# Performance work log

Hardware: AMD Instinct MI355X
Metric: run time of the kernel (lower is better)

## Reference

```python
import jax, jax.numpy as jnp
import numpy as np

EPS = 1e-5

def _bn(h, gamma, beta):
    # BatchNorm1d in training mode: batch stats over dim 0, biased variance
    mu = h.mean(axis=0)
    var = ((h - mu) ** 2).mean(axis=0)
    return gamma * (h - mu) * jax.lax.rsqrt(var + EPS) + beta

def _gnn_layer(x, w, src, dst, Wv, bv, We, be, g_n, b_n, g_e, b_e):
    n_nodes = x.shape[0]
    # 4 node linears: Wv [4,d,d], bv [4,d]
    xl = jnp.einsum('nd,kfd->knf', x, Wv) + bv[:, None, :]  # [4, N, d]
    x1, x2, x3, x4 = xl[0], xl[1], xl[2], xl[3]
    # sigmoid-gated messages, mean-aggregated to source nodes
    msg = jax.nn.sigmoid(w) * x2[dst]                         # [E, d]
    agg = jax.ops.segment_sum(msg, src, num_segments=n_nodes)
    cnt = jax.ops.segment_sum(jnp.ones((src.shape[0], 1), x.dtype), src,
                              num_segments=n_nodes)
    agg = agg / jnp.maximum(cnt, 1.0)
    x_new = x + jax.nn.silu(_bn(x1 + agg, g_n, b_n))
    w_new = w + jax.nn.silu(_bn(w @ We.T + be + x3[src] + x4[dst], g_e, b_e))
    return x_new, w_new

def setup_inputs() -> dict:
    key = jax.random.key(0)
    N, E, D, L = 50000, 800000, 64, 3
    ks = jax.random.split(key, 10)
    x = jax.random.normal(ks[0], (N, D), dtype=jnp.float32)
    edge_index = jax.random.randint(ks[1], (2, E), 0, N, dtype=jnp.int64)
    edge_attr = jax.random.normal(ks[2], (E, D), dtype=jnp.float32)
    Wv = jax.random.normal(ks[3], (L, 4, D, D), dtype=jnp.float32) * 0.05
    bv = jax.random.normal(ks[4], (L, 4, D), dtype=jnp.float32) * 0.05
    We = jax.random.normal(ks[5], (L, D, D), dtype=jnp.float32) * 0.05
    be = jax.random.normal(ks[6], (L, D), dtype=jnp.float32) * 0.05
    g_node = jnp.ones((L, D), dtype=jnp.float32)
    b_node = jnp.zeros((L, D), dtype=jnp.float32)
    g_edge = jnp.ones((L, D), dtype=jnp.float32)
    b_edge = jnp.zeros((L, D), dtype=jnp.float32)
    return {"x": x, "edge_index": edge_index, "edge_attr": edge_attr,
            "Wv": Wv, "bv": bv, "We": We, "be": be,
            "g_node": g_node, "b_node": b_node,
            "g_edge": g_edge, "b_edge": b_edge}

def reference(x, edge_index, edge_attr, Wv, bv, We, be,
              g_node, b_node, g_edge, b_edge):
    src, dst = edge_index[0], edge_index[1]
    h = jax.nn.silu(x)
    w = jax.nn.silu(edge_attr)
    L = Wv.shape[0]
    for l in range(L):
        h, w = _gnn_layer(h, w, src, dst, Wv[l], bv[l], We[l], be[l],
                          g_node[l], b_node[l], g_edge[l], b_edge[l])
    return h, w
```

## Files before the change

kernel.cpp:

```cpp
#include <hip/hip_runtime.h>

#define NN 50000
#define NE 800000
#define EPSB 1e-5f

typedef __attribute__((ext_vector_type(8))) short bf16x8;
typedef __attribute__((ext_vector_type(8))) unsigned short ushort8;
typedef __attribute__((ext_vector_type(4))) float f32x4;

__device__ __forceinline__ float sigm(float x){ return 1.0f/(1.0f+__expf(-x)); }
__device__ __forceinline__ float silu_(float x){ return x/(1.0f+__expf(-x)); }
__device__ __forceinline__ unsigned int cvt2(float lo, float hi){
  unsigned int r;
  asm("v_cvt_pk_bf16_f32 %0, %1, %2" : "=v"(r) : "v"(lo), "v"(hi));
  return r;
}
__device__ __forceinline__ unsigned short f2bf(float x){
  return (unsigned short)cvt2(x, 0.f);
}
__device__ __forceinline__ float bf2f(unsigned short b){
  return __uint_as_float(((unsigned int)b)<<16);
}
__device__ __forceinline__ ushort8 pack8(float a0,float a1,float a2,float a3,
                                         float a4,float a5,float a6,float a7){
  union { unsigned int u[4]; ushort8 s; } z;
  z.u[0]=cvt2(a0,a1); z.u[1]=cvt2(a2,a3); z.u[2]=cvt2(a4,a5); z.u[3]=cvt2(a6,a7);
  return z.s;
}
__device__ __forceinline__ ushort8 sum8(ushort8 a, ushort8 b){
  return pack8(bf2f(a[0])+bf2f(b[0]), bf2f(a[1])+bf2f(b[1]),
               bf2f(a[2])+bf2f(b[2]), bf2f(a[3])+bf2f(b[3]),
               bf2f(a[4])+bf2f(b[4]), bf2f(a[5])+bf2f(b[5]),
               bf2f(a[6])+bf2f(b[6]), bf2f(a[7])+bf2f(b[7]));
}


__global__ __launch_bounds__(256) void k_deg(const int* __restrict__ src,
                                             int* __restrict__ deg){
  int e = blockIdx.x*256 + threadIdx.x;
  if (e < NE) atomicAdd(&deg[src[e]], 1);
}

__global__ __launch_bounds__(1024) void k_scan(const int* __restrict__ deg,
    int* __restrict__ cursor, float* __restrict__ invd){
  __shared__ int wsum[16];
  __shared__ int sbase;
  if (threadIdx.x == 0) sbase = 0;
  __syncthreads();
  const int lane = threadIdx.x & 63, wid = threadIdx.x >> 6;
  for (int start = 0; start < NN; start += 1024){
    int n = start + (int)threadIdx.x;
    int v = (n < NN) ? deg[n] : 0;
    int x = v;
    #pragma unroll
    for (int d=1; d<64; d<<=1){
      int y = __shfl_up(x, d);
      if (lane >= d) x += y;
    }
    if (lane == 63) wsum[wid] = x;
    __syncthreads();
    if (threadIdx.x < 16){
      int s = wsum[threadIdx.x];
      #pragma unroll
      for (int d=1; d<16; d<<=1){
        int y = __shfl_up(s, d);
        if ((int)threadIdx.x >= d) s += y;
      }
      wsum[threadIdx.x] = s;
    }
    __syncthreads();
    int excl = sbase + ((wid>0)? wsum[wid-1] : 0) + (x - v);
    if (n < NN){
      cursor[n] = excl;
      invd[n] = 1.0f / fmaxf((float)v, 1.0f);
    }
    __syncthreads();
    if (threadIdx.x == 0) sbase += wsum[15];
    __syncthreads();
  }
}

__global__ __launch_bounds__(256) void k_scatter(const int* __restrict__ src,
    const int* __restrict__ dst, int* __restrict__ cursor,
    int* __restrict__ perm, int* __restrict__ ssrc, int* __restrict__ sdst){
  int e = blockIdx.x*256 + threadIdx.x;
  if (e < NE){
    int s = src[e];
    int pos = atomicAdd(&cursor[s], 1);
    perm[pos] = e;
    ssrc[pos] = s;
    sdst[pos] = dst[e];
  }
}

__global__ __launch_bounds__(256) void k_prepW(const float* __restrict__ Wv,
    const float* __restrict__ We,
    unsigned short* __restrict__ wvs, unsigned short* __restrict__ wes){
  const int m = blockIdx.x;
  const float* S = (m < 12) ? (Wv + m*4096) : (We + (m-12)*4096);
  unsigned short* O = (m < 12) ? (wvs + m*4096) : (wes + (m-12)*4096);
  int t = threadIdx.x;
  #pragma unroll
  for (int p=0; p<2; ++p){
    int c = t + p*256;
    int row = c>>3, cc = c&7;
    const float4* sp = (const float4*)(S + row*64 + cc*8);
    float4 a = sp[0], b = sp[1];
    ushort8 v = pack8(a.x,a.y,a.z,a.w,b.x,b.y,b.z,b.w);
    *(ushort8*)((char*)O + ((row*128 + cc*16) ^ ((row&7)<<4))) = v;
  }
}

template<int MODE>
__global__ __launch_bounds__(256) void k_nodelin(const float* __restrict__ xin,
    float* __restrict__ h, float* __restrict__ x1, float* __restrict__ agg,
    const float* __restrict__ invd, const float* __restrict__ coefp,
    const unsigned short* __restrict__ wvs, const float* __restrict__ bvl,
    unsigned short* __restrict__ xb){
  __shared__ unsigned short shb[4096];
  __shared__ unsigned short sW[4096];
  const int n0 = blockIdx.x*64;
  const int t = threadIdx.x;
  #pragma unroll
  for (int p=0; p<2; ++p){
    int c = t + p*256;
    int row = c>>3, cc = c&7;
    int n = n0 + row;
    ushort8 v = {0,0,0,0,0,0,0,0};
    if (n < NN){
      unsigned base = (unsigned)n*64u + (unsigned)cc*8u;
      float4 a, b;
      if (MODE == 0){
        const float4* xp = (const float4*)(xin + base);
        a = xp[0]; b = xp[1];
        a.x=silu_(a.x); a.y=silu_(a.y); a.z=silu_(a.z); a.w=silu_(a.w);
        b.x=silu_(b.x); b.y=silu_(b.y); b.z=silu_(b.z); b.w=silu_(b.w);
        float4* hp = (float4*)(h + base);
        hp[0] = a; hp[1] = b;
      } else {
        float4* hp = (float4*)(h + base);
        a = hp[0]; b = hp[1];
        const float4* xp = (const float4*)(x1 + base);
        float4* gp = (float4*)(agg + base);
        float iv = invd[n];
        float4 xa = xp[0], xb4 = xp[1], ga = gp[0], gb = gp[1];
        float4 z = make_float4(0.f,0.f,0.f,0.f);
        gp[0] = z; gp[1] = z;
        float4 s0 = *(const float4*)(coefp + cc*8);
        float4 s1v = *(const float4*)(coefp + cc*8 + 4);
        float4 h0 = *(const float4*)(coefp + 64 + cc*8);
        float4 h1 = *(const float4*)(coefp + 64 + cc*8 + 4);
        a.x += silu_((xa.x + ga.x*iv)*s0.x + h0.x);
        a.y += silu_((xa.y + ga.y*iv)*s0.y + h0.y);
        a.z += silu_((xa.z + ga.z*iv)*s0.z + h0.z);
        a.w += silu_((xa.w + ga.w*iv)*s0.w + h0.w);
        b.x += silu_((xb4.x + gb.x*iv)*s1v.x + h1.x);
        b.y += silu_((xb4.y + gb.y*iv)*s1v.y + h1.y);
        b.z += silu_((xb4.z + gb.z*iv)*s1v.z + h1.z);
        b.w += silu_((xb4.w + gb.w*iv)*s1v.w + h1.w);
        hp[0] = a; hp[1] = b;
      }
      v = pack8(a.x,a.y,a.z,a.w,b.x,b.y,b.z,b.w);
    }
    *(ushort8*)((char*)shb + ((row*128 + cc*16) ^ ((row&7)<<4))) = v;
  }
  __syncthreads();
  const int wid = t>>6, lane = t&63, g = lane>>4, ln = lane&15;
  const int arow = wid*16 + ln;
  bf16x8 afr0 = *(bf16x8*)((char*)shb + ((arow*128 +  0 + g*16) ^ ((arow&7)<<4)));
  bf16x8 afr1 = *(bf16x8*)((char*)shb + ((arow*128 + 64 + g*16) ^ ((arow&7)<<4)));
  for (int k=0; k<4; ++k){
    __syncthreads();
    ((ushort8*)sW)[t]     = ((const ushort8*)(wvs + k*4096))[t];
    ((ushort8*)sW)[t+256] = ((const ushort8*)(wvs + k*4096))[t+256];
    __syncthreads();
    #pragma unroll
    for (int ft=0; ft<4; ++ft){
      int brow = ft*16 + ln;
      bf16x8 b0 = *(bf16x8*)((char*)sW + ((brow*128 +  0 + g*16) ^ ((brow&7)<<4)));
      bf16x8 b1 = *(bf16x8*)((char*)sW + ((brow*128 + 64 + g*16) ^ ((brow&7)<<4)));
      f32x4 c = {0.f,0.f,0.f,0.f};
      c = __builtin_amdgcn_mfma_f32_16x16x32_bf16(afr0, b0, c, 0,0,0);
      c = __builtin_amdgcn_mfma_f32_16x16x32_bf16(afr1, b1, c, 0,0,0);
      float bias = bvl[k*64 + brow];
      #pragma unroll
      for (int r=0; r<4; ++r){
        int n = n0 + wid*16 + g*4 + r;
        if (n < NN){
          float val = c[r] + bias;
          unsigned off = (unsigned)n*64u + (unsigned)brow;
          if (k == 0) x1[off] = val;
          else xb[(unsigned)(k-1)*(NN*64u) + off] = f2bf(val);
        }
      }
    }
  }
}

template<int FIRST>
__global__ __launch_bounds__(256) void k_edgeA(const float* __restrict__ ea,
    unsigned short* __restrict__ wb16,
    const int* __restrict__ perm, const int* __restrict__ ssrc,
    const int* __restrict__ sdst,
    const unsigned short* __restrict__ wesO, const unsigned short* __restrict__ wesN,
    const float* __restrict__ beO, const float* __restrict__ beN,
    const unsigned short* __restrict__ x3o, const unsigned short* __restrict__ x4o,
    const unsigned short* __restrict__ x2n, const unsigned short* __restrict__ x3n,
    const unsigned short* __restrict__ x4n, const float* __restrict__ coefp,
    float* __restrict__ agg, float* __restrict__ esum, float* __restrict__ esq){
  __shared__ unsigned short sWb[4096];
  __shared__ unsigned short swb[4096];
  __shared__ unsigned short sxs[4096];
  __shared__ int sidx[128];
  const int e0 = blockIdx.x*64;
  const unsigned ebase = (unsigned)e0*64u;
  const int t = threadIdx.x;
  const int row0 = t>>3, cc8 = t&7, rr1 = row0+32;
  const int wid = t>>6, lane = t&63, g = lane>>4, ln = lane&15;
  const int arow = wid*16 + ln;

  unsigned sA0=(unsigned)ssrc[e0+row0], dA0=(unsigned)sdst[e0+row0];
  unsigned sA1=(unsigned)ssrc[e0+rr1],  dA1=(unsigned)sdst[e0+rr1];

  if (t < 64) sidx[t] = ssrc[e0+t];
  else if (t < 128) sidx[t] = sdst[e0+t-64];

  {
    const unsigned short* wesP = FIRST ? wesN : wesO;
    ((ushort8*)sWb)[t]     = ((const ushort8*)wesP)[t];
    ((ushort8*)sWb)[t+256] = ((const ushort8*)wesP)[t+256];
  }
  #pragma unroll
  for (int p=0; p<2; ++p){
    int c = t + p*256;
    int row = row0 + p*32;
    ushort8 v;
    if (FIRST){
      unsigned esrc = (unsigned)perm[e0 + row];
      const float4* sp = (const float4*)(ea + esrc*64u + (unsigned)cc8*8u);
      float4 a = sp[0], b = sp[1];
      v = pack8(silu_(a.x),silu_(a.y),silu_(a.z),silu_(a.w),
                silu_(b.x),silu_(b.y),silu_(b.z),silu_(b.w));
      ((ushort8*)(wb16 + ebase))[c] = v;
    } else {
      v = ((const ushort8*)(wb16 + ebase))[c];
    }
    *(ushort8*)((char*)swb + ((row*128 + cc8*16) ^ ((row&7)<<4))) = v;
  }
  {
    const unsigned short* X3 = FIRST ? x3n : x3o;
    const unsigned short* X4 = FIRST ? x4n : x4o;
    ushort8 a0 = *(const ushort8*)(X3 + sA0*64u + (unsigned)cc8*8u);
    ushort8 b0 = *(const ushort8*)(X4 + dA0*64u + (unsigned)cc8*8u);
    ushort8 a1 = *(const ushort8*)(X3 + sA1*64u + (unsigned)cc8*8u);
    ushort8 b1 = *(const ushort8*)(X4 + dA1*64u + (unsigned)cc8*8u);
    *(ushort8*)((char*)sxs + ((row0*128 + cc8*16) ^ ((row0&7)<<4))) = sum8(a0,b0);
    *(ushort8*)((char*)sxs + ((rr1*128  + cc8*16) ^ ((rr1&7)<<4)))  = sum8(a1,b1);
  }
  __syncthreads();

  if (!FIRST){
    bf16x8 afr0 = *(bf16x8*)((char*)swb + ((arow*128 +  0 + g*16) ^ ((arow&7)<<4)));
    bf16x8 afr1 = *(bf16x8*)((char*)swb + ((arow*128 + 64 + g*16) ^ ((arow&7)<<4)));
    bf16x8 bfr[4][2];
    #pragma unroll
    for (int ft=0; ft<4; ++ft){
      int brow = ft*16 + ln;
      bfr[ft][0] = *(bf16x8*)((char*)sWb + ((brow*128 +  0 + g*16) ^ ((brow&7)<<4)));
      bfr[ft][1] = *(bf16x8*)((char*)sWb + ((brow*128 + 64 + g*16) ^ ((brow&7)<<4)));
    }
    f32x4 cacc[4];
    #pragma unroll
    for (int ft=0; ft<4; ++ft){
      f32x4 c = {0.f,0.f,0.f,0.f};
      c = __builtin_amdgcn_mfma_f32_16x16x32_bf16(afr0, bfr[ft][0], c, 0,0,0);
      c = __builtin_amdgcn_mfma_f32_16x16x32_bf16(afr1, bfr[ft][1], c, 0,0,0);
      cacc[ft] = c;
    }
    float scp[4], shp[4], beo[4], wnew[4][4];
    #pragma unroll
    for (int ft=0; ft<4; ++ft){
      scp[ft] = coefp[128 + ft*16 + ln];
      shp[ft] = coefp[192 + ft*16 + ln];
      beo[ft] = beO[ft*16 + ln];
    }
    #pragma unroll
    for (int r=0; r<4; ++r){
      int row = wid*16 + g*4 + r;
      #pragma unroll
      for (int ft=0; ft<4; ++ft){
        int f = ft*16 + ln;
        unsigned short a34 = *(unsigned short*)((char*)sxs + ((row*128 + f*2) ^ ((row&7)<<4)));
        unsigned short wo  = *(unsigned short*)((char*)swb + ((row*128 + f*2) ^ ((row&7)<<4)));
        float u = cacc[ft][r] + beo[ft] + bf2f(a34);
        wnew[ft][r] = bf2f(wo) + silu_(u*scp[ft] + shp[ft]);
      }
    }
    __syncthreads();

    #pragma unroll
    for (int r=0; r<4; ++r){
      int row = wid*16 + g*4 + r;
      #pragma unroll
      for (int ft=0; ft<4; ++ft){
        int f = ft*16 + ln;
        *(unsigned short*)((char*)swb + ((row*128 + f*2) ^ ((row&7)<<4))) = f2bf(wnew[ft][r]);
      }
    }
    ((ushort8*)sWb)[t]     = ((const ushort8*)wesN)[t];
    ((ushort8*)sWb)[t+256] = ((const ushort8*)wesN)[t+256];
    {
      ushort8 a0 = *(const ushort8*)(x3n + sA0*64u + (unsigned)cc8*8u);
      ushort8 b0 = *(const ushort8*)(x4n + dA0*64u + (unsigned)cc8*8u);
      ushort8 a1 = *(const ushort8*)(x3n + sA1*64u + (unsigned)cc8*8u);
      ushort8 b1 = *(const ushort8*)(x4n + dA1*64u + (unsigned)cc8*8u);
      *(ushort8*)((char*)sxs + ((row0*128 + cc8*16) ^ ((row0&7)<<4))) = sum8(a0,b0);
      *(ushort8*)((char*)sxs + ((rr1*128  + cc8*16) ^ ((rr1&7)<<4)))  = sum8(a1,b1);
    }
    __syncthreads();

    #pragma unroll
    for (int p=0; p<2; ++p){
      int c = t + p*256;
      int row = row0 + p*32;
      ushort8 v = *(ushort8*)((char*)swb + ((row*128 + cc8*16) ^ ((row&7)<<4)));
      ((ushort8*)(wb16 + ebase))[c] = v;
    }
  }

  bf16x8 afr0 = *(bf16x8*)((char*)swb + ((arow*128 +  0 + g*16) ^ ((arow&7)<<4)));
  bf16x8 afr1 = *(bf16x8*)((char*)swb + ((arow*128 + 64 + g*16) ^ ((arow&7)<<4)));
  bf16x8 bfr[4][2];
  #pragma unroll
  for (int ft=0; ft<4; ++ft){
    int brow = ft*16 + ln;
    bfr[ft][0] = *(bf16x8*)((char*)sWb + ((brow*128 +  0 + g*16) ^ ((brow&7)<<4)));
    bfr[ft][1] = *(bf16x8*)((char*)sWb + ((brow*128 + 64 + g*16) ^ ((brow&7)<<4)));
  }
  f32x4 cacc[4];
  #pragma unroll
  for (int ft=0; ft<4; ++ft){
    f32x4 c = {0.f,0.f,0.f,0.f};
    c = __builtin_amdgcn_mfma_f32_16x16x32_bf16(afr0, bfr[ft][0], c, 0,0,0);
    c = __builtin_amdgcn_mfma_f32_16x16x32_bf16(afr1, bfr[ft][1], c, 0,0,0);
    cacc[ft] = c;
  }
  float ben[4], s1[4]={0.f,0.f,0.f,0.f}, s2[4]={0.f,0.f,0.f,0.f};
  #pragma unroll
  for (int ft=0; ft<4; ++ft) ben[ft] = beN[ft*16+ln];
  #pragma unroll
  for (int r=0; r<4; ++r){
    int row = wid*16 + g*4 + r;
    #pragma unroll
    for (int ft=0; ft<4; ++ft){
      int f = ft*16 + ln;
      unsigned short a34 = *(unsigned short*)((char*)sxs + ((row*128 + f*2) ^ ((row&7)<<4)));
      float u = cacc[ft][r] + ben[ft] + bf2f(a34);
      s1[ft] += u; s2[ft] += u*u;
    }
  }
  #pragma unroll
  for (int ft=0; ft<4; ++ft){
    s1[ft] += __shfl_xor(s1[ft], 16); s1[ft] += __shfl_xor(s1[ft], 32);
    s2[ft] += __shfl_xor(s2[ft], 16); s2[ft] += __shfl_xor(s2[ft], 32);
  }
  if (g == 0){
    int slot = ((blockIdx.x<<2) + wid) & 63;
    #pragma unroll
    for (int ft=0; ft<4; ++ft){
      atomicAdd(&esum[(slot<<6) + ft*16 + ln], s1[ft]);
      atomicAdd(&esq [(slot<<6) + ft*16 + ln], s2[ft]);
    }
  }
  __syncthreads();

  {
    ushort8 v0 = *(const ushort8*)(x2n + dA0*64u + (unsigned)cc8*8u);
    ushort8 v1 = *(const ushort8*)(x2n + dA1*64u + (unsigned)cc8*8u);
    *(ushort8*)((char*)sxs + ((row0*128 + cc8*16) ^ ((row0&7)<<4))) = v0;
    *(ushort8*)((char*)sxs + ((rr1*128  + cc8*16) ^ ((rr1&7)<<4)))  = v1;
  }
  __syncthreads();

  {
    const int el0 = wid<<4;
    unsigned curs = (unsigned)sidx[el0];
    float run = 0.f;
    #pragma unroll
    for (int j=0; j<16; ++j){
      int el = el0 + j;
      unsigned s = (unsigned)sidx[el];
      if (s != curs){
        atomicAdd(&agg[curs*64u + (unsigned)lane], run);
        run = 0.f; curs = s;
      }
      unsigned short wv = *(unsigned short*)((char*)swb + ((el*128 + lane*2) ^ ((el&7)<<4)));
      unsigned short xv = *(unsigned short*)((char*)sxs + ((el*128 + lane*2) ^ ((el&7)<<4)));
      run += sigm(bf2f(wv)) * bf2f(xv);
    }
    atomicAdd(&agg[curs*64u + (unsigned)lane], run);
  }
}

__global__ __launch_bounds__(256) void k_edgeFin(const unsigned short* __restrict__ wb16,
    const int* __restrict__ perm, const int* __restrict__ ssrc,
    const int* __restrict__ sdst,
    const unsigned short* __restrict__ wes2, const float* __restrict__ be2,
    const unsigned short* __restrict__ x3c, const unsigned short* __restrict__ x4c,
    const float* __restrict__ coef2, float* __restrict__ wout){
  __shared__ unsigned short sWb[4096];
  __shared__ unsigned short swb[4096];
  __shared__ unsigned short sxs[4096];
  const int e0 = blockIdx.x*64;
  const unsigned ebase = (unsigned)e0*64u;
  const int t = threadIdx.x;
  const int row0 = t>>3, cc8 = t&7, rr1 = row0+32;
  const int wid = t>>6, lane = t&63, g = lane>>4, ln = lane&15;
  const int arow = wid*16 + ln;

  unsigned sA0=(unsigned)ssrc[e0+row0], dA0=(unsigned)sdst[e0+row0];
  unsigned sA1=(unsigned)ssrc[e0+rr1],  dA1=(unsigned)sdst[e0+rr1];

  ((ushort8*)sWb)[t]     = ((const ushort8*)wes2)[t];
  ((ushort8*)sWb)[t+256] = ((const ushort8*)wes2)[t+256];
  #pragma unroll
  for (int p=0; p<2; ++p){
    int c = t + p*256;
    int row = row0 + p*32;
    ushort8 v = ((const ushort8*)(wb16 + ebase))[c];
    *(ushort8*)((char*)swb + ((row*128 + cc8*16) ^ ((row&7)<<4))) = v;
  }
  {
    ushort8 a0 = *(const ushort8*)(x3c + sA0*64u + (unsigned)cc8*8u);
    ushort8 b0 = *(const ushort8*)(x4c + dA0*64u + (unsigned)cc8*8u);
    ushort8 a1 = *(const ushort8*)(x3c + sA1*64u + (unsigned)cc8*8u);
    ushort8 b1 = *(const ushort8*)(x4c + dA1*64u + (unsigned)cc8*8u);
    *(ushort8*)((char*)sxs + ((row0*128 + cc8*16) ^ ((row0&7)<<4))) = sum8(a0,b0);
    *(ushort8*)((char*)sxs + ((rr1*128  + cc8*16) ^ ((rr1&7)<<4)))  = sum8(a1,b1);
  }
  __syncthreads();

  bf16x8 afr0 = *(bf16x8*)((char*)swb + ((arow*128 +  0 + g*16) ^ ((arow&7)<<4)));
  bf16x8 afr1 = *(bf16x8*)((char*)swb + ((arow*128 + 64 + g*16) ^ ((arow&7)<<4)));
  bf16x8 bfr[4][2];
  #pragma unroll
  for (int ft=0; ft<4; ++ft){
    int brow = ft*16 + ln;
    bfr[ft][0] = *(bf16x8*)((char*)sWb + ((brow*128 +  0 + g*16) ^ ((brow&7)<<4)));
    bfr[ft][1] = *(bf16x8*)((char*)sWb + ((brow*128 + 64 + g*16) ^ ((brow&7)<<4)));
  }
  f32x4 cacc[4];
  #pragma unroll
  for (int ft=0; ft<4; ++ft){
    f32x4 c = {0.f,0.f,0.f,0.f};
    c = __builtin_amdgcn_mfma_f32_16x16x32_bf16(afr0, bfr[ft][0], c, 0,0,0);
    c = __builtin_amdgcn_mfma_f32_16x16x32_bf16(afr1, bfr[ft][1], c, 0,0,0);
    cacc[ft] = c;
  }
  float scp[4], shp[4], be4[4];
  #pragma unroll
  for (int ft=0; ft<4; ++ft){
    scp[ft] = coef2[128 + ft*16 + ln];
    shp[ft] = coef2[192 + ft*16 + ln];
    be4[ft] = be2[ft*16 + ln];
  }
  #pragma unroll
  for (int r=0; r<4; ++r){
    int row = wid*16 + g*4 + r;
    #pragma unroll
    for (int ft=0; ft<4; ++ft){
      int f = ft*16 + ln;
      unsigned short* slot = (unsigned short*)((char*)sxs + ((row*128 + f*2) ^ ((row&7)<<4)));
      unsigned short wo = *(unsigned short*)((char*)swb + ((row*128 + f*2) ^ ((row&7)<<4)));
      float u = cacc[ft][r] + be4[ft] + bf2f(*slot);
      float o = bf2f(wo) + silu_(u*scp[ft] + shp[ft]);
      *slot = f2bf(o);
    }
  }
  __syncthreads();

  #pragma unroll
  for (int p=0; p<2; ++p){
    int c = t + p*256;
    int row = row0 + p*32;
    ushort8 v = *(ushort8*)((char*)sxs + ((row*128 + cc8*16) ^ ((row&7)<<4)));
    unsigned eid = (unsigned)perm[e0 + row];
    float4 oa = make_float4(bf2f(v[0]),bf2f(v[1]),bf2f(v[2]),bf2f(v[3]));
    float4 ob = make_float4(bf2f(v[4]),bf2f(v[5]),bf2f(v[6]),bf2f(v[7]));
    float4* wp = (float4*)(wout + eid*64u + (unsigned)cc8*8u);
    wp[0] = oa; wp[1] = ob;
  }
}

__global__ __launch_bounds__(256) void k_nodestats(const float* __restrict__ x1,
    const float* __restrict__ agg, const float* __restrict__ invd,
    float* __restrict__ nsum, float* __restrict__ nsq){
  const int f = threadIdx.x & 63, sub = threadIdx.x >> 6;
  float s1=0.f, s2=0.f;
  for (int n = blockIdx.x*4 + sub; n < NN; n += gridDim.x*4){
    unsigned off = (unsigned)n*64u + (unsigned)f;
    float t = x1[off] + agg[off]*invd[n];
    s1 += t; s2 += t*t;
  }
  __shared__ float red[4][64][2];
  red[sub][f][0]=s1; red[sub][f][1]=s2;
  __syncthreads();
  if (sub==0){
    float a1=red[0][f][0]+red[1][f][0]+red[2][f][0]+red[3][f][0];
    float a2=red[0][f][1]+red[1][f][1]+red[2][f][1]+red[3][f][1];
    int slot = blockIdx.x & 63;
    atomicAdd(&nsum[(slot<<6)+f], a1);
    atomicAdd(&nsq[(slot<<6)+f], a2);
  }
}

__global__ void k_finalize(float* __restrict__ nsum, float* __restrict__ nsq,
    float* __restrict__ esum, float* __restrict__ esq,
    const float* __restrict__ gn, const float* __restrict__ bn,
    const float* __restrict__ ge, const float* __restrict__ beb,
    float* __restrict__ coef){
  int t = threadIdx.x;
  if (t >= 128) return;
  int f = t & 63;
  float* S1 = (t<64)? nsum : esum;
  float* S2 = (t<64)? nsq  : esq;
  float cnt = (t<64)? (float)NN : (float)NE;
  float s1=0.f, s2=0.f;
  for (int k=0;k<64;++k){ s1 += S1[(k<<6)+f]; s2 += S2[(k<<6)+f]; }
  for (int k=0;k<64;++k){ S1[(k<<6)+f]=0.f; S2[(k<<6)+f]=0.f; }
  float mu = s1/cnt;
  float var = s2/cnt - mu*mu;
  float rstd = rsqrtf(var + EPSB);
  float g = (t<64)? gn[f] : ge[f];
  float b = (t<64)? bn[f] : beb[f];
  float sc = g*rstd, sh = b - mu*sc;
  coef[((t<64)?0:2)*64 + f] = sc;
  coef[((t<64)?1:3)*64 + f] = sh;
}

__global__ __launch_bounds__(256) void k_nodeupd(const float* __restrict__ x1,
    const float* __restrict__ agg, const float* __restrict__ invd,
    const float* __restrict__ coef, float* __restrict__ h){
  unsigned i = blockIdx.x*256u + threadIdx.x;
  if (i >= NN*64u) return;
  unsigned n = i>>6, f = i&63u;
  float t = x1[i] + agg[i]*invd[n];
  float v = t*coef[f] + coef[64+f];
  h[i] += silu_(v);
}


extern "C" void kernel_launch(void* const* d_in, const int* in_sizes, int n_in,
                              void* d_out, int out_size, void* d_ws, size_t ws_size,
                              hipStream_t stream){
  const float* x      = (const float*)d_in[0];
  const int*   eidx   = (const int*)d_in[1];
  const float* eattr  = (const float*)d_in[2];
  const float* Wv     = (const float*)d_in[3];
  const float* bv     = (const float*)d_in[4];
  const float* We     = (const float*)d_in[5];
  const float* be     = (const float*)d_in[6];
  const float* g_node = (const float*)d_in[7];
  const float* b_node = (const float*)d_in[8];
  const float* g_edge = (const float*)d_in[9];
  const float* b_edge = (const float*)d_in[10];
  const int* src = eidx;
  const int* dst = eidx + NE;

  float* hout = (float*)d_out;
  float* wout = hout + (size_t)NN*64;

  float* W    = (float*)d_ws;
  float* x1   = W;
  float* agg  = W + 3200000;
  float* nsum = W + 6400000;
  float* nsq  = W + 6404096;
  float* esum = W + 6408192;
  float* esq  = W + 6412288;
  float* coef = W + 6416384;
  float* invd = W + 6417152;
  int*   deg  = (int*)(W + 6467152);
  unsigned short* xb   = (unsigned short*)(W + 6517152);
  unsigned short* wvs  = (unsigned short*)(W + 16200000);
  unsigned short* wes  = (unsigned short*)(W + 16230000);
  unsigned short* wb16 = (unsigned short*)(W + 16240000);
  int* perm   = (int*)(W + 41840000);
  int* ssrc   = (int*)(W + 42640000);
  int* sdst   = (int*)(W + 43440000);
  int* cursor = (int*)(W + 44240000);

  hipMemsetAsync(deg, 0, NN*sizeof(int), stream);
  hipMemsetAsync(agg, 0, (3200000 + 4*4096)*sizeof(float), stream);
  k_deg<<<3125, 256, 0, stream>>>(src, deg);
  k_scan<<<1, 1024, 0, stream>>>(deg, cursor, invd);
  k_scatter<<<3125, 256, 0, stream>>>(src, dst, cursor, perm, ssrc, sdst);
  k_prepW<<<15, 256, 0, stream>>>(Wv, We, wvs, wes);

  const unsigned N64 = NN*64u;
  for (int l=0; l<3; ++l){
    int gc = l & 1, go = (l-1) & 1;
    unsigned short* xbc = xb + (size_t)gc*3*N64;
    unsigned short* xbo = xb + (size_t)go*3*N64;
    const float* cprev = coef + (l-1)*256;
    if (l == 0)
      k_nodelin<0><<<782, 256, 0, stream>>>(x, hout, x1, agg, invd, coef,
          wvs + l*16384, bv + l*256, xbc);
    else
      k_nodelin<1><<<782, 256, 0, stream>>>(x, hout, x1, agg, invd, cprev,
          wvs + l*16384, bv + l*256, xbc);
    if (l == 0)
      k_edgeA<1><<<12500, 256, 0, stream>>>(eattr, wb16, perm, ssrc, sdst,
          wes, wes, be, be,
          xbo + N64, xbo + 2*N64,
          xbc, xbc + N64, xbc + 2*N64,
          coef, agg, esum, esq);
    else
      k_edgeA<0><<<12500, 256, 0, stream>>>(eattr, wb16, perm, ssrc, sdst,
          wes + (l-1)*4096, wes + l*4096, be + (l-1)*64, be + l*64,
          xbo + N64, xbo + 2*N64,
          xbc, xbc + N64, xbc + 2*N64,
          cprev, agg, esum, esq);
    k_nodestats<<<128, 256, 0, stream>>>(x1, agg, invd, nsum, nsq);
    k_finalize<<<1, 128, 0, stream>>>(nsum, nsq, esum, esq,
        g_node + l*64, b_node + l*64, g_edge + l*64, b_edge + l*64, coef + l*256);
  }
  unsigned short* xb2 = xb;
  k_nodeupd<<<12500, 256, 0, stream>>>(x1, agg, invd, coef + 512, hout);
  k_edgeFin<<<12500, 256, 0, stream>>>(wb16, perm, ssrc, sdst,
      wes + 2*4096, be + 2*64, xb2 + N64, xb2 + 2*N64, coef + 512, wout);
}
```

Measured before the change: 768.9 us.

## Interleave x2/x4 per node and make edge kernels persistent grid-stride

Node linear outputs x4 and x2 are now stored interleaved in one 128-wide per-node row, so the dst-indexed gathers in the edge kernel touch one contiguous region per node. The edge kernels become persistent: 1024 blocks loop over the 12500 tiles, loading the We weights and per-feature coefficients into shared memory once per block rather than once per tile. The nodestats grid is also doubled. This adds extra barriers per tile iteration and a second We buffer in shared memory, which may reduce occupancy.

After: 834.5 us. +8.5%, slower.

```diff
diff --git a/kernel.cpp b/kernel.cpp
--- a/kernel.cpp
+++ b/kernel.cpp
@@ -3,6 +3,7 @@
 #define NN 50000
 #define NE 800000
 #define EPSB 1e-5f
+#define NTILE 12500
 
 typedef __attribute__((ext_vector_type(8))) short bf16x8;
 typedef __attribute__((ext_vector_type(8))) unsigned short ushort8;
@@ -116,7 +117,7 @@
     float* __restrict__ h, float* __restrict__ x1, float* __restrict__ agg,
     const float* __restrict__ invd, const float* __restrict__ coefp,
     const unsigned short* __restrict__ wvs, const float* __restrict__ bvl,
-    unsigned short* __restrict__ xb){
+    unsigned short* __restrict__ x3T, unsigned short* __restrict__ dstT){
   __shared__ unsigned short shb[4096];
   __shared__ unsigned short sW[4096];
   const int n0 = blockIdx.x*64;
@@ -188,9 +189,10 @@
         int n = n0 + wid*16 + g*4 + r;
         if (n < NN){
           float val = c[r] + bias;
-          unsigned off = (unsigned)n*64u + (unsigned)brow;
-          if (k == 0) x1[off] = val;
-          else xb[(unsigned)(k-1)*(NN*64u) + off] = f2bf(val);
+          if (k == 0)      x1 [(unsigned)n*64u  + (unsigned)brow] = val;
+          else if (k == 1) dstT[(unsigned)n*128u + 64u + (unsigned)brow] = f2bf(val);
+          else if (k == 2) x3T[(unsigned)n*64u  + (unsigned)brow] = f2bf(val);
+          else             dstT[(unsigned)n*128u + (unsigned)brow] = f2bf(val);
         }
       }
     }
@@ -204,201 +206,202 @@
     const int* __restrict__ sdst,
     const unsigned short* __restrict__ wesO, const unsigned short* __restrict__ wesN,
     const float* __restrict__ beO, const float* __restrict__ beN,
-    const unsigned short* __restrict__ x3o, const unsigned short* __restrict__ x4o,
-    const unsigned short* __restrict__ x2n, const unsigned short* __restrict__ x3n,
-    const unsigned short* __restrict__ x4n, const float* __restrict__ coefp,
+    const unsigned short* __restrict__ x3o, const unsigned short* __restrict__ dstO,
+    const unsigned short* __restrict__ x3n, const unsigned short* __restrict__ dstN,
+    const float* __restrict__ coefp,
     float* __restrict__ agg, float* __restrict__ esum, float* __restrict__ esq){
-  __shared__ unsigned short sWb[4096];
+  __shared__ unsigned short sWeO[4096], sWeN[4096];
   __shared__ unsigned short swb[4096];
   __shared__ unsigned short sxs[4096];
   __shared__ int sidx[128];
-  const int e0 = blockIdx.x*64;
-  const unsigned ebase = (unsigned)e0*64u;
   const int t = threadIdx.x;
   const int row0 = t>>3, cc8 = t&7, rr1 = row0+32;
   const int wid = t>>6, lane = t&63, g = lane>>4, ln = lane&15;
   const int arow = wid*16 + ln;
 
-  unsigned sA0=(unsigned)ssrc[e0+row0], dA0=(unsigned)sdst[e0+row0];
-  unsigned sA1=(unsigned)ssrc[e0+rr1],  dA1=(unsigned)sdst[e0+rr1];
-
-  if (t < 64) sidx[t] = ssrc[e0+t];
-  else if (t < 128) sidx[t] = sdst[e0+t-64];
-
-  {
-    const unsigned short* wesP = FIRST ? wesN : wesO;
-    ((ushort8*)sWb)[t]     = ((const ushort8*)wesP)[t];
-    ((ushort8*)sWb)[t+256] = ((const ushort8*)wesP)[t+256];
-  }
+  if (!FIRST){
+    ((ushort8*)sWeO)[t]     = ((const ushort8*)wesO)[t];
+    ((ushort8*)sWeO)[t+256] = ((const ushort8*)wesO)[t+256];
+  }
+  ((ushort8*)sWeN)[t]     = ((const ushort8*)wesN)[t];
+  ((ushort8*)sWeN)[t+256] = ((const ushort8*)wesN)[t+256];
+
+  float scp[4], shp[4], beo[4], ben[4];
   #pragma unroll
-  for (int p=0; p<2; ++p){
-    int c = t + p*256;
-    int row = row0 + p*32;
-    ushort8 v;
-    if (FIRST){
-      unsigned esrc = (unsigned)perm[e0 + row];
-      const float4* sp = (const float4*)(ea + esrc*64u + (unsigned)cc8*8u);
-      float4 a = sp[0], b = sp[1];
-      v = pack8(silu_(a.x),silu_(a.y),silu_(a.z),silu_(a.w),
-                silu_(b.x),silu_(b.y),silu_(b.z),silu_(b.w));
-      ((ushort8*)(wb16 + ebase))[c] = v;
-    } else {
-      v = ((const ushort8*)(wb16 + ebase))[c];
-    }
-    *(ushort8*)((char*)swb + ((row*128 + cc8*16) ^ ((row&7)<<4))) = v;
-  }
-  {
-    const unsigned short* X3 = FIRST ? x3n : x3o;
-    const unsigned short* X4 = FIRST ? x4n : x4o;
-    ushort8 a0 = *(const ushort8*)(X3 + sA0*64u + (unsigned)cc8*8u);
-    ushort8 b0 = *(const ushort8*)(X4 + dA0*64u + (unsigned)cc8*8u);
-    ushort8 a1 = *(const ushort8*)(X3 + sA1*64u + (unsigned)cc8*8u);
-    ushort8 b1 = *(const ushort8*)(X4 + dA1*64u + (unsigned)cc8*8u);
-    *(ushort8*)((char*)sxs + ((row0*128 + cc8*16) ^ ((row0&7)<<4))) = sum8(a0,b0);
-    *(ushort8*)((char*)sxs + ((rr1*128  + cc8*16) ^ ((rr1&7)<<4)))  = sum8(a1,b1);
-  }
-  __syncthreads();
-
-  if (!FIRST){
-    bf16x8 afr0 = *(bf16x8*)((char*)swb + ((arow*128 +  0 + g*16) ^ ((arow&7)<<4)));
-    bf16x8 afr1 = *(bf16x8*)((char*)swb + ((arow*128 + 64 + g*16) ^ ((arow&7)<<4)));
-    bf16x8 bfr[4][2];
-    #pragma unroll
-    for (int ft=0; ft<4; ++ft){
-      int brow = ft*16 + ln;
-      bfr[ft][0] = *(bf16x8*)((char*)sWb + ((brow*128 +  0 + g*16) ^ ((brow&7)<<4)));
-      bfr[ft][1] = *(bf16x8*)((char*)sWb + ((brow*128 + 64 + g*16) ^ ((brow&7)<<4)));
-    }
-    f32x4 cacc[4];
-    #pragma unroll
-    for (int ft=0; ft<4; ++ft){
-      f32x4 c = {0.f,0.f,0.f,0.f};
-      c = __builtin_amdgcn_mfma_f32_16x16x32_bf16(afr0, bfr[ft][0], c, 0,0,0);
-      c = __builtin_amdgcn_mfma_f32_16x16x32_bf16(afr1, bfr[ft][1], c, 0,0,0);
-      cacc[ft] = c;
-    }
-    float scp[4], shp[4], beo[4], wnew[4][4];
-    #pragma unroll
-    for (int ft=0; ft<4; ++ft){
+  for (int ft=0; ft<4; ++ft){
+    ben[ft] = beN[ft*16+ln];
+    if (!FIRST){
       scp[ft] = coefp[128 + ft*16 + ln];
       shp[ft] = coefp[192 + ft*16 + ln];
       beo[ft] = beO[ft*16 + ln];
     }
-    #pragma unroll
-    for (int r=0; r<4; ++r){
-      int row = wid*16 + g*4 + r;
-      #pragma unroll
-      for (int ft=0; ft<4; ++ft){
-        int f = ft*16 + ln;
-        unsigned short a34 = *(unsigned short*)((char*)sxs + ((row*128 + f*2) ^ ((row&7)<<4)));
-        unsigned short wo  = *(unsigned short*)((char*)swb + ((row*128 + f*2) ^ ((row&7)<<4)));
-        float u = cacc[ft][r] + beo[ft] + bf2f(a34);
-        wnew[ft][r] = bf2f(wo) + silu_(u*scp[ft] + shp[ft]);
-      }
-    }
-    __syncthreads();
-
-    #pragma unroll
-    for (int r=0; r<4; ++r){
-      int row = wid*16 + g*4 + r;
-      #pragma unroll
-      for (int ft=0; ft<4; ++ft){
-        int f = ft*16 + ln;
-        *(unsigned short*)((char*)swb + ((row*128 + f*2) ^ ((row&7)<<4))) = f2bf(wnew[ft][r]);
-      }
-    }
-    ((ushort8*)sWb)[t]     = ((const ushort8*)wesN)[t];
-    ((ushort8*)sWb)[t+256] = ((const ushort8*)wesN)[t+256];
-    {
-      ushort8 a0 = *(const ushort8*)(x3n + sA0*64u + (unsigned)cc8*8u);
-      ushort8 b0 = *(const ushort8*)(x4n + dA0*64u + (unsigned)cc8*8u);
-      ushort8 a1 = *(const ushort8*)(x3n + sA1*64u + (unsigned)cc8*8u);
-      ushort8 b1 = *(const ushort8*)(x4n + dA1*64u + (unsigned)cc8*8u);
-      *(ushort8*)((char*)sxs + ((row0*128 + cc8*16) ^ ((row0&7)<<4))) = sum8(a0,b0);
-      *(ushort8*)((char*)sxs + ((rr1*128  + cc8*16) ^ ((rr1&7)<<4)))  = sum8(a1,b1);
-    }
-    __syncthreads();
+  }
+
+  for (int tile = blockIdx.x; tile < NTILE; tile += gridDim.x){
+    const int e0 = tile*64;
+    const unsigned ebase = (unsigned)e0*64u;
+    __syncthreads();
+
+    if (t < 64) sidx[t] = ssrc[e0+t];
+    else if (t < 128) sidx[t] = sdst[e0+t-64];
+    unsigned sA0=(unsigned)ssrc[e0+row0], dA0=(unsigned)sdst[e0+row0];
+    unsigned sA1=(unsigned)ssrc[e0+rr1],  dA1=(unsigned)sdst[e0+rr1];
 
     #pragma unroll
     for (int p=0; p<2; ++p){
       int c = t + p*256;
       int row = row0 + p*32;
-      ushort8 v = *(ushort8*)((char*)swb + ((row*128 + cc8*16) ^ ((row&7)<<4)));
-      ((ushort8*)(wb16 + ebase))[c] = v;
-    }
-  }
-
-  bf16x8 afr0 = *(bf16x8*)((char*)swb + ((arow*128 +  0 + g*16) ^ ((arow&7)<<4)));
-  bf16x8 afr1 = *(bf16x8*)((char*)swb + ((arow*128 + 64 + g*16) ^ ((arow&7)<<4)));
-  bf16x8 bfr[4][2];
-  #pragma unroll
-  for (int ft=0; ft<4; ++ft){
-    int brow = ft*16 + ln;
-    bfr[ft][0] = *(bf16x8*)((char*)sWb + ((brow*128 +  0 + g*16) ^ ((brow&7)<<4)));
-    bfr[ft][1] = *(bf16x8*)((char*)sWb + ((brow*128 + 64 + g*16) ^ ((brow&7)<<4)));
-  }
-  f32x4 cacc[4];
-  #pragma unroll
-  for (int ft=0; ft<4; ++ft){
-    f32x4 c = {0.f,0.f,0.f,0.f};
-    c = __builtin_amdgcn_mfma_f32_16x16x32_bf16(afr0, bfr[ft][0], c, 0,0,0);
-    c = __builtin_amdgcn_mfma_f32_16x16x32_bf16(afr1, bfr[ft][1], c, 0,0,0);
-    cacc[ft] = c;
-  }
-  float ben[4], s1[4]={0.f,0.f,0.f,0.f}, s2[4]={0.f,0.f,0.f,0.f};
-  #pragma unroll
-  for (int ft=0; ft<4; ++ft) ben[ft] = beN[ft*16+ln];
-  #pragma unroll
-  for (int r=0; r<4; ++r){
-    int row = wid*16 + g*4 + r;
-    #pragma unroll
-    for (int ft=0; ft<4; ++ft){
-      int f = ft*16 + ln;
-      unsigned short a34 = *(unsigned short*)((char*)sxs + ((row*128 + f*2) ^ ((row&7)<<4)));
-      float u = cacc[ft][r] + ben[ft] + bf2f(a34);
-      s1[ft] += u; s2[ft] += u*u;
-    }
-  }
-  #pragma unroll
-  for (int ft=0; ft<4; ++ft){
-    s1[ft] += __shfl_xor(s1[ft], 16); s1[ft] += __shfl_xor(s1[ft], 32);
-    s2[ft] += __shfl_xor(s2[ft], 16); s2[ft] += __shfl_xor(s2[ft], 32);
-  }
-  if (g == 0){
-    int slot = ((blockIdx.x<<2) + wid) & 63;
-    #pragma unroll
-    for (int ft=0; ft<4; ++ft){
-      atomicAdd(&esum[(slot<<6) + ft*16 + ln], s1[ft]);
-      atomicAdd(&esq [(slot<<6) + ft*16 + ln], s2[ft]);
-    }
-  }
-  __syncthreads();
-
-  {
-    ushort8 v0 = *(const ushort8*)(x2n + dA0*64u + (unsigned)cc8*8u);
-    ushort8 v1 = *(const ushort8*)(x2n + dA1*64u + (unsigned)cc8*8u);
-    *(ushort8*)((char*)sxs + ((row0*128 + cc8*16) ^ ((row0&7)<<4))) = v0;
-    *(ushort8*)((char*)sxs + ((rr1*128  + cc8*16) ^ ((rr1&7)<<4)))  = v1;
-  }
-  __syncthreads();
-
-  {
-    const int el0 = wid<<4;
-    unsigned curs = (unsigned)sidx[el0];
-    float run = 0.f;
-    #pragma unroll
-    for (int j=0; j<16; ++j){
-      int el = el0 + j;
-      unsigned s = (unsigned)sidx[el];
-      if (s != curs){
-        atomicAdd(&agg[curs*64u + (unsigned)lane], run);
-        run = 0.f; curs = s;
-      }
-      unsigned short wv = *(unsigned short*)((char*)swb + ((el*128 + lane*2) ^ ((el&7)<<4)));
-      unsigned short xv = *(unsigned short*)((char*)sxs + ((el*128 + lane*2) ^ ((el&7)<<4)));
-      run += sigm(bf2f(wv)) * bf2f(xv);
-    }
-    atomicAdd(&agg[curs*64u + (unsigned)lane], run);
+      ushort8 v;
+      if (FIRST){
+        unsigned esrc = (unsigned)perm[e0 + row];
+        const float4* sp = (const float4*)(ea + esrc*64u + (unsigned)cc8*8u);
+        float4 a = sp[0], b = sp[1];
+        v = pack8(silu_(a.x),silu_(a.y),silu_(a.z),silu_(a.w),
+                  silu_(b.x),silu_(b.y),silu_(b.z),silu_(b.w));
+        ((ushort8*)(wb16 + ebase))[c] = v;
+      } else {
+        v = ((const ushort8*)(wb16 + ebase))[c];
+      }
+      *(ushort8*)((char*)swb + ((row*128 + cc8*16) ^ ((row&7)<<4))) = v;
+    }
+    {
+      const unsigned short* X3 = FIRST ? x3n : x3o;
+      const unsigned short* DT = FIRST ? dstN : dstO;
+      ushort8 a0 = *(const ushort8*)(X3 + sA0*64u  + (unsigned)cc8*8u);
+      ushort8 b0 = *(const ushort8*)(DT + dA0*128u + (unsigned)cc8*8u);
+      ushort8 a1 = *(const ushort8*)(X3 + sA1*64u  + (unsigned)cc8*8u);
+      ushort8 b1 = *(const ushort8*)(DT + dA1*128u + (unsigned)cc8*8u);
+      *(ushort8*)((char*)sxs + ((row0*128 + cc8*16) ^ ((row0&7)<<4))) = sum8(a0,b0);
+      *(ushort8*)((char*)sxs + ((rr1*128  + cc8*16) ^ ((rr1&7)<<4)))  = sum8(a1,b1);
+    }
+    __syncthreads();
+
+    if (!FIRST){
+      bf16x8 afr0 = *(bf16x8*)((char*)swb + ((arow*128 +  0 + g*16) ^ ((arow&7)<<4)));
+      bf16x8 afr1 = *(bf16x8*)((char*)swb + ((arow*128 + 64 + g*16) ^ ((arow&7)<<4)));
+      f32x4 cacc[4];
+      #pragma unroll
+      for (int ft=0; ft<4; ++ft){
+        int brow = ft*16 + ln;
+        bf16x8 b0 = *(bf16x8*)((char*)sWeO + ((brow*128 +  0 + g*16) ^ ((brow&7)<<4)));
+        bf16x8 b1 = *(bf16x8*)((char*)sWeO + ((brow*128 + 64 + g*16) ^ ((brow&7)<<4)));
+        f32x4 c = {0.f,0.f,0.f,0.f};
+        c = __builtin_amdgcn_mfma_f32_16x16x32_bf16(afr0, b0, c, 0,0,0);
+        c = __builtin_amdgcn_mfma_f32_16x16x32_bf16(afr1, b1, c, 0,0,0);
+        cacc[ft] = c;
+      }
+      float wnew[4][4];
+      #pragma unroll
+      for (int r=0; r<4; ++r){
+        int row = wid*16 + g*4 + r;
+        #pragma unroll
+        for (int ft=0; ft<4; ++ft){
+          int f = ft*16 + ln;
+          unsigned short a34 = *(unsigned short*)((char*)sxs + ((row*128 + f*2) ^ ((row&7)<<4)));
+          unsigned short wo  = *(unsigned short*)((char*)swb + ((row*128 + f*2) ^ ((row&7)<<4)));
+          float u = cacc[ft][r] + beo[ft] + bf2f(a34);
+          wnew[ft][r] = bf2f(wo) + silu_(u*scp[ft] + shp[ft]);
+        }
+      }
+      __syncthreads();
+
+      #pragma unroll
+      for (int r=0; r<4; ++r){
+        int row = wid*16 + g*4 + r;
+        #pragma unroll
+        for (int ft=0; ft<4; ++ft){
+          int f = ft*16 + ln;
+          *(unsigned short*)((char*)swb + ((row*128 + f*2) ^ ((row&7)<<4))) = f2bf(wnew[ft][r]);
+        }
+      }
+      {
+        ushort8 a0 = *(const ushort8*)(x3n + sA0*64u  + (unsigned)cc8*8u);
+        ushort8 b0 = *(const ushort8*)(dstN + dA0*128u + (unsigned)cc8*8u);
+        ushort8 a1 = *(const ushort8*)(x3n + sA1*64u  + (unsigned)cc8*8u);
+        ushort8 b1 = *(const ushort8*)(dstN + dA1*128u + (unsigned)cc8*8u);
+        *(ushort8*)((char*)sxs + ((row0*128 + cc8*16) ^ ((row0&7)<<4))) = sum8(a0,b0);
+        *(ushort8*)((char*)sxs + ((rr1*128  + cc8*16) ^ ((rr1&7)<<4)))  = sum8(a1,b1);
+      }
+      __syncthreads();
+
+      #pragma unroll
+      for (int p=0; p<2; ++p){
+        int c = t + p*256;
+        int row = row0 + p*32;
+        ushort8 v = *(ushort8*)((char*)swb + ((row*128 + cc8*16) ^ ((row&7)<<4)));
+        ((ushort8*)(wb16 + ebase))[c] = v;
+      }
+    }
+
+    {
+      bf16x8 afr0 = *(bf16x8*)((char*)swb + ((arow*128 +  0 + g*16) ^ ((arow&7)<<4)));
+      bf16x8 afr1 = *(bf16x8*)((char*)swb + ((arow*128 + 64 + g*16) ^ ((arow&7)<<4)));
+      f32x4 cacc[4];
+      #pragma unroll
+      for (int ft=0; ft<4; ++ft){
+        int brow = ft*16 + ln;
+        bf16x8 b0 = *(bf16x8*)((char*)sWeN + ((brow*128 +  0 + g*16) ^ ((brow&7)<<4)));
+        bf16x8 b1 = *(bf16x8*)((char*)sWeN + ((brow*128 + 64 + g*16) ^ ((brow&7)<<4)));
+        f32x4 c = {0.f,0.f,0.f,0.f};
+        c = __builtin_amdgcn_mfma_f32_16x16x32_bf16(afr0, b0, c, 0,0,0);
+        c = __builtin_amdgcn_mfma_f32_16x16x32_bf16(afr1, b1, c, 0,0,0);
+        cacc[ft] = c;
+      }
+      float s1[4]={0.f,0.f,0.f,0.f}, s2[4]={0.f,0.f,0.f,0.f};
+      #pragma unroll
+      for (int r=0; r<4; ++r){
+        int row = wid*16 + g*4 + r;
+        #pragma unroll
+        for (int ft=0; ft<4; ++ft){
+          int f = ft*16 + ln;
+          unsigned short a34 = *(unsigned short*)((char*)sxs + ((row*128 + f*2) ^ ((row&7)<<4)));
+          float u = cacc[ft][r] + ben[ft] + bf2f(a34);
+          s1[ft] += u; s2[ft] += u*u;
+        }
+      }
+      #pragma unroll
+      for (int ft=0; ft<4; ++ft){
+        s1[ft] += __shfl_xor(s1[ft], 16); s1[ft] += __shfl_xor(s1[ft], 32);
+        s2[ft] += __shfl_xor(s2[ft], 16); s2[ft] += __shfl_xor(s2[ft], 32);
+      }
+      if (g == 0){
+        int slot = ((tile<<2) + wid) & 63;
+        #pragma unroll
+        for (int ft=0; ft<4; ++ft){
+          atomicAdd(&esum[(slot<<6) + ft*16 + ln], s1[ft]);
+          atomicAdd(&esq [(slot<<6) + ft*16 + ln], s2[ft]);
+        }
+      }
+    }
+    __syncthreads();
+
+    {
+      const unsigned short* DT = dstN;
+      ushort8 v0 = *(const ushort8*)(DT + dA0*128u + 64u + (unsigned)cc8*8u);
+      ushort8 v1 = *(const ushort8*)(DT + dA1*128u + 64u + (unsigned)cc8*8u);
+      *(ushort8*)((char*)sxs + ((row0*128 + cc8*16) ^ ((row0&7)<<4))) = v0;
+      *(ushort8*)((char*)sxs + ((rr1*128  + cc8*16) ^ ((rr1&7)<<4)))  = v1;
+    }
+    __syncthreads();
+
+    {
+      const int el0 = wid<<4;
+      unsigned curs = (unsigned)sidx[el0];
+      float run = 0.f;
+      #pragma unroll
+      for (int j=0; j<16; ++j){
+        int el = el0 + j;
+        unsigned s = (unsigned)sidx[el];
+        if (s != curs){
+          atomicAdd(&agg[curs*64u + (unsigned)lane], run);
+          run = 0.f; curs = s;
+        }
+        unsigned short wv = *(unsigned short*)((char*)swb + ((el*128 + lane*2) ^ ((el&7)<<4)));
+        unsigned short xv = *(unsigned short*)((char*)sxs + ((el*128 + lane*2) ^ ((el&7)<<4)));
+        run += sigm(bf2f(wv)) * bf2f(xv);
+      }
+      atomicAdd(&agg[curs*64u + (unsigned)lane], run);
+    }
   }
 }
 
@@ -406,57 +409,18 @@
     const int* __restrict__ perm, const int* __restrict__ ssrc,
     const int* __restrict__ sdst,
     const unsigned short* __restrict__ wes2, const float* __restrict__ be2,
-    const unsigned short* __restrict__ x3c, const unsigned short* __restrict__ x4c,
+    const unsigned short* __restrict__ x3c, const unsigned short* __restrict__ dstC,
     const float* __restrict__ coef2, float* __restrict__ wout){
-  __shared__ unsigned short sWb[4096];
+  __shared__ unsigned short sWe[4096];
   __shared__ unsigned short swb[4096];
   __shared__ unsigned short sxs[4096];
-  const int e0 = blockIdx.x*64;
-  const unsigned ebase = (unsigned)e0*64u;
   const int t = threadIdx.x;
   const int row0 = t>>3, cc8 = t&7, rr1 = row0+32;
   const int wid = t>>6, lane = t&63, g = lane>>4, ln = lane&15;
   const int arow = wid*16 + ln;
 
-  unsigned sA0=(unsigned)ssrc[e0+row0], dA0=(unsigned)sdst[e0+row0];
-  unsigned sA1=(unsigned)ssrc[e0+rr1],  dA1=(unsigned)sdst[e0+rr1];
-
-  ((ushort8*)sWb)[t]     = ((const ushort8*)wes2)[t];
-  ((ushort8*)sWb)[t+256] = ((const ushort8*)wes2)[t+256];
-  #pragma unroll
-  for (int p=0; p<2; ++p){
-    int c = t + p*256;
-    int row = row0 + p*32;
-    ushort8 v = ((const ushort8*)(wb16 + ebase))[c];
-    *(ushort8*)((char*)swb + ((row*128 + cc8*16) ^ ((row&7)<<4))) = v;
-  }
-  {
-    ushort8 a0 = *(const ushort8*)(x3c + sA0*64u + (unsigned)cc8*8u);
-    ushort8 b0 = *(const ushort8*)(x4c + dA0*64u + (unsigned)cc8*8u);
-    ushort8 a1 = *(const ushort8*)(x3c + sA1*64u + (unsigned)cc8*8u);
-    ushort8 b1 = *(const ushort8*)(x4c + dA1*64u + (unsigned)cc8*8u);
-    *(ushort8*)((char*)sxs + ((row0*128 + cc8*16) ^ ((row0&7)<<4))) = sum8(a0,b0);
-    *(ushort8*)((char*)sxs + ((rr1*128  + cc8*16) ^ ((rr1&7)<<4)))  = sum8(a1,b1);
-  }
-  __syncthreads();
-
-  bf16x8 afr0 = *(bf16x8*)((char*)swb + ((arow*128 +  0 + g*16) ^ ((arow&7)<<4)));
-  bf16x8 afr1 = *(bf16x8*)((char*)swb + ((arow*128 + 64 + g*16) ^ ((arow&7)<<4)));
-  bf16x8 bfr[4][2];
-  #pragma unroll
-  for (int ft=0; ft<4; ++ft){
-    int brow = ft*16 + ln;
-    bfr[ft][0] = *(bf16x8*)((char*)sWb + ((brow*128 +  0 + g*16) ^ ((brow&7)<<4)));
-    bfr[ft][1] = *(bf16x8*)((char*)sWb + ((brow*128 + 64 + g*16) ^ ((brow&7)<<4)));
-  }
-  f32x4 cacc[4];
-  #pragma unroll
-  for (int ft=0; ft<4; ++ft){
-    f32x4 c = {0.f,0.f,0.f,0.f};
-    c = __builtin_amdgcn_mfma_f32_16x16x32_bf16(afr0, bfr[ft][0], c, 0,0,0);
-    c = __builtin_amdgcn_mfma_f32_16x16x32_bf16(afr1, bfr[ft][1], c, 0,0,0);
-    cacc[ft] = c;
-  }
+  ((ushort8*)sWe)[t]     = ((const ushort8*)wes2)[t];
+  ((ushort8*)sWe)[t+256] = ((const ushort8*)wes2)[t+256];
   float scp[4], shp[4], be4[4];
   #pragma unroll
   for (int ft=0; ft<4; ++ft){
@@ -464,31 +428,71 @@
     shp[ft] = coef2[192 + ft*16 + ln];
     be4[ft] = be2[ft*16 + ln];
   }
-  #pragma unroll
-  for (int r=0; r<4; ++r){
-    int row = wid*16 + g*4 + r;
+
+  for (int tile = blockIdx.x; tile < NTILE; tile += gridDim.x){
+    const int e0 = tile*64;
+    const unsigned ebase = (unsigned)e0*64u;
+    __syncthreads();
+
+    unsigned sA0=(unsigned)ssrc[e0+row0], dA0=(unsigned)sdst[e0+row0];
+    unsigned sA1=(unsigned)ssrc[e0+rr1],  dA1=(unsigned)sdst[e0+rr1];
+
+    #pragma unroll
+    for (int p=0; p<2; ++p){
+      int c = t + p*256;
+      int row = row0 + p*32;
+      ushort8 v = ((const ushort8*)(wb16 + ebase))[c];
+      *(ushort8*)((char*)swb + ((row*128 + cc8*16) ^ ((row&7)<<4))) = v;
+    }
+    {
+      ushort8 a0 = *(const ushort8*)(x3c + sA0*64u  + (unsigned)cc8*8u);
+      ushort8 b0 = *(const ushort8*)(dstC + dA0*128u + (unsigned)cc8*8u);
+      ushort8 a1 = *(const ushort8*)(x3c + sA1*64u  + (unsigned)cc8*8u);
+      ushort8 b1 = *(const ushort8*)(dstC + dA1*128u + (unsigned)cc8*8u);
+      *(ushort8*)((char*)sxs + ((row0*128 + cc8*16) ^ ((row0&7)<<4))) = sum8(a0,b0);
+      *(ushort8*)((char*)sxs + ((rr1*128  + cc8*16) ^ ((rr1&7)<<4)))  = sum8(a1,b1);
+    }
+    __syncthreads();
+
+    bf16x8 afr0 = *(bf16x8*)((char*)swb + ((arow*128 +  0 + g*16) ^ ((arow&7)<<4)));
+    bf16x8 afr1 = *(bf16x8*)((char*)swb + ((arow*128 + 64 + g*16) ^ ((arow&7)<<4)));
+    f32x4 cacc[4];
     #pragma unroll
     for (int ft=0; ft<4; ++ft){
-      int f = ft*16 + ln;
-      unsigned short* slot = (unsigned short*)((char*)sxs + ((row*128 + f*2) ^ ((row&7)<<4)));
-      unsigned short wo = *(unsigned short*)((char*)swb + ((row*128 + f*2) ^ ((row&7)<<4)));
-      float u = cacc[ft][r] + be4[ft] + bf2f(*slot);
-      float o = bf2f(wo) + silu_(u*scp[ft] + shp[ft]);
-      *slot = f2bf(o);
-    }
-  }
-  __syncthreads();
-
-  #pragma unroll
-  for (int p=0; p<2; ++p){
-    int c = t + p*256;
-    int row = row0 + p*32;
-    ushort8 v = *(ushort8*)((char*)sxs + ((row*128 + cc8*16) ^ ((row&7)<<4)));
-    unsigned eid = (unsigned)perm[e0 + row];
-    float4 oa = make_float4(bf2f(v[0]),bf2f(v[1]),bf2f(v[2]),bf2f(v[3]));
-    float4 ob = make_float4(bf2f(v[4]),bf2f(v[5]),bf2f(v[6]),bf2f(v[7]));
-    float4* wp = (float4*)(wout + eid*64u + (unsigned)cc8*8u);
-    wp[0] = oa; wp[1] = ob;
+      int brow = ft*16 + ln;
+      bf16x8 b0 = *(bf16x8*)((char*)sWe + ((brow*128 +  0 + g*16) ^ ((brow&7)<<4)));
+      bf16x8 b1 = *(bf16x8*)((char*)sWe + ((brow*128 + 64 + g*16) ^ ((brow&7)<<4)));
+      f32x4 c = {0.f,0.f,0.f,0.f};
+      c = __builtin_amdgcn_mfma_f32_16x16x32_bf16(afr0, b0, c, 0,0,0);
+      c = __builtin_amdgcn_mfma_f32_16x16x32_bf16(afr1, b1, c, 0,0,0);
+      cacc[ft] = c;
+    }
+    #pragma unroll
+    for (int r=0; r<4; ++r){
+      int row = wid*16 + g*4 + r;
+      #pragma unroll
+      for (int ft=0; ft<4; ++ft){
+        int f = ft*16 + ln;
+        unsigned short* slot = (unsigned short*)((char*)sxs + ((row*128 + f*2) ^ ((row&7)<<4)));
+        unsigned short wo = *(unsigned short*)((char*)swb + ((row*128 + f*2) ^ ((row&7)<<4)));
+        float u = cacc[ft][r] + be4[ft] + bf2f(*slot);
+        float o = bf2f(wo) + silu_(u*scp[ft] + shp[ft]);
+        *slot = f2bf(o);
+      }
+    }
+    __syncthreads();
+
+    #pragma unroll
+    for (int p=0; p<2; ++p){
+      int c = t + p*256;
+      int row = row0 + p*32;
+      ushort8 v = *(ushort8*)((char*)sxs + ((row*128 + cc8*16) ^ ((row&7)<<4)));
+      unsigned eid = (unsigned)perm[e0 + row];
+      float4 oa = make_float4(bf2f(v[0]),bf2f(v[1]),bf2f(v[2]),bf2f(v[3]));
+      float4 ob = make_float4(bf2f(v[4]),bf2f(v[5]),bf2f(v[6]),bf2f(v[7]));
+      float4* wp = (float4*)(wout + eid*64u + (unsigned)cc8*8u);
+      wp[0] = oa; wp[1] = ob;
+    }
   }
 }
 
@@ -601,31 +605,33 @@
     int gc = l & 1, go = (l-1) & 1;
     unsigned short* xbc = xb + (size_t)gc*3*N64;
     unsigned short* xbo = xb + (size_t)go*3*N64;
+    unsigned short* x3c = xbc,      * dtc = xbc + N64;
+    unsigned short* x3o = xbo,      * dto = xbo + N64;
     const float* cprev = coef + (l-1)*256;
     if (l == 0)
       k_nodelin<0><<<782, 256, 0, stream>>>(x, hout, x1, agg, invd, coef,
-          wvs + l*16384, bv + l*256, xbc);
+          wvs + l*16384, bv + l*256, x3c, dtc);
     else
       k_nodelin<1><<<782, 256, 0, stream>>>(x, hout, x1, agg, invd, cprev,
-          wvs + l*16384, bv + l*256, xbc);
+          wvs + l*16384, bv + l*256, x3c, dtc);
     if (l == 0)
-      k_edgeA<1><<<12500, 256, 0, stream>>>(eattr, wb16, perm, ssrc, sdst,
+      k_edgeA<1><<<1024, 256, 0, stream>>>(eattr, wb16, perm, ssrc, sdst,
           wes, wes, be, be,
-          xbo + N64, xbo + 2*N64,
-          xbc, xbc + N64, xbc + 2*N64,
+          x3o, dto,
+          x3c, dtc,
           coef, agg, esum, esq);
     else
-      k_edgeA<0><<<12500, 256, 0, stream>>>(eattr, wb16, perm, ssrc, sdst,
+      k_edgeA<0><<<1024, 256, 0, stream>>>(eattr, wb16, perm, ssrc, sdst,
           wes + (l-1)*4096, wes + l*4096, be + (l-1)*64, be + l*64,
-          xbo + N64, xbo + 2*N64,
-          xbc, xbc + N64, xbc + 2*N64,
+          x3o, dto,
+          x3c, dtc,
           cprev, agg, esum, esq);
-    k_nodestats<<<128, 256, 0, stream>>>(x1, agg, invd, nsum, nsq);
+    k_nodestats<<<256, 256, 0, stream>>>(x1, agg, invd, nsum, nsq);
     k_finalize<<<1, 128, 0, stream>>>(nsum, nsq, esum, esq,
         g_node + l*64, b_node + l*64, g_edge + l*64, b_edge + l*64, coef + l*256);
   }
   unsigned short* xb2 = xb;
   k_nodeupd<<<12500, 256, 0, stream>>>(x1, agg, invd, coef + 512, hout);
-  k_edgeFin<<<12500, 256, 0, stream>>>(wb16, perm, ssrc, sdst,
-      wes + 2*4096, be + 2*64, xb2 + N64, xb2 + 2*N64, coef + 512, wout);
-}
+  k_edgeFin<<<1024, 256, 0, stream>>>(wb16, perm, ssrc, sdst,
+      wes + 2*4096, be + 2*64, xb2, xb2 + N64, coef + 512, wout);
+}
```
